# Performance work log

Measured on AMD Instinct MI355X. Metric: run time of the kernel, lower is better.

## Reference

```python
import jax, jax.numpy as jnp
import numpy as np

N, B, NG = 12288, 8, 1536   # total nodes, graphs, nodes per graph
E, T, R, H = 49152, 9, 4, 128  # edges, node types, edge types, hidden

def setup_inputs() -> dict:
    key = jax.random.key(0)
    ks = jax.random.split(key, 24)
    s = 0.05
    inp = {
        'n_feats': jax.random.uniform(ks[0], (N, T), jnp.float32),
        'eps': jax.random.normal(ks[1], (N, H), jnp.float32),
        'edge_src': jax.random.randint(ks[2], (E,), 0, N, jnp.int32),
        'edge_dst': jax.random.randint(ks[3], (E,), 0, N, jnp.int32),
        'e_types': jax.random.randint(ks[4], (E,), 0, R, jnp.int32),
        # RelGraphConv params: per-relation weight, self-loop weight, bias
        'W1': jax.random.normal(ks[5], (R, T, H)) * s,  'Ws1': jax.random.normal(ks[6], (T, H)) * s,  'b1': jnp.zeros((H,)),
        'W2': jax.random.normal(ks[7], (R, H, H)) * s,  'Ws2': jax.random.normal(ks[8], (H, H)) * s,  'b2': jnp.zeros((H,)),
        'Wmu': jax.random.normal(ks[9], (R, H, H)) * s, 'Wsmu': jax.random.normal(ks[10], (H, H)) * s, 'bmu': jnp.zeros((H,)),
        'Wls': jax.random.normal(ks[11], (R, H, H)) * s, 'Wsls': jax.random.normal(ks[12], (H, H)) * s, 'bls': jnp.zeros((H,)),
        # decoder heads
        'Wnt': jax.random.normal(ks[13], (H, T)) * s, 'bnt': jnp.zeros((T,)),
        'we': jax.random.normal(ks[14], (3 * H + 2 * T,)) * s, 'be': jnp.zeros(()),
        'Wt': jax.random.normal(ks[15], (3 * H + 2 * T, R)) * s, 'bt': jnp.zeros((R,)),
    }
    return inp

def _relconv(h, W, Wself, b, edge_src, edge_dst, e_types):
    # per-relation transform then gather per edge: avoids [E,d,d] weight gather
    hr = jnp.einsum('nd,rdk->rnk', h, W)          # [R,N,H]
    msgs = hr[e_types, edge_src]                   # [E,H]
    agg = jax.ops.segment_sum(msgs, edge_dst, num_segments=N)
    return agg + h @ Wself + b

def reference(n_feats, eps, edge_src, edge_dst, e_types,
              W1, Ws1, b1, W2, Ws2, b2, Wmu, Wsmu, bmu, Wls, Wsls, bls,
              Wnt, bnt, we, be, Wt, bt):
    # ---- encode ----
    h = jax.nn.relu(_relconv(n_feats, W1, Ws1, b1, edge_src, edge_dst, e_types))
    h = jax.nn.relu(_relconv(h, W2, Ws2, b2, edge_src, edge_dst, e_types))
    mu = _relconv(h, Wmu, Wsmu, bmu, edge_src, edge_dst, e_types)
    logstd = _relconv(h, Wls, Wsls, bls, edge_src, edge_dst, e_types)
    z = mu + eps * jnp.exp(logstd)                 # reparameterize
    gz = z.reshape(B, NG, H).mean(axis=1)          # per-graph mean readout [B,H]

    # ---- decode (batched pairwise MLP) ----
    nt = z @ Wnt + bnt                             # [N,T]
    # edge_existence_fc on concat(u_z,u_t,v_z,v_t,gz) decomposes rank-1:
    wu_z, wu_t = we[:H], we[H:H + T]
    wv_z, wv_t = we[H + T:2 * H + T], we[2 * H + T:2 * H + 2 * T]
    wg = we[2 * H + 2 * T:]
    su = (z @ wu_z + nt @ wu_t).reshape(B, NG)     # [B,n]
    sv = (z @ wv_z + nt @ wv_t).reshape(B, NG)
    sg = gz @ wg + be                              # [B]
    exist = jax.nn.sigmoid(su[:, :, None] + sv[:, None, :] + sg[:, None, None])  # [B,n,n]

    Au = (z @ Wt[:H] + nt @ Wt[H:H + T]).reshape(B, NG, R)
    Av = (z @ Wt[H + T:2 * H + T] + nt @ Wt[2 * H + T:2 * H + 2 * T]).reshape(B, NG, R)
    Ag = gz @ Wt[2 * H + 2 * T:] + bt              # [B,R]
    type_logits = Au[:, :, None, :] + Av[:, None, :, :] + Ag[:, None, None, :]  # [B,n,n,R]

    pair_out = jnp.concatenate([exist[..., None], type_logits], axis=-1)  # [B,n,n,1+R]
    return pair_out, nt, mu, logstd
```

## Files before the change

### kernel.cpp

```cpp
#include <hip/hip_runtime.h>

#define NN 12288
#define TT 9
#define RR 4
#define HH 128
#define EE 49152
#define BB 8
#define NGG 1536
#define CAP 16

typedef unsigned short u16;
typedef float float4_t __attribute__((ext_vector_type(4)));
typedef __bf16 bf16x8 __attribute__((ext_vector_type(8)));
typedef unsigned short ushort8_t __attribute__((ext_vector_type(8)));

__device__ __forceinline__ u16 f2bf(float f) {
    union { float f; unsigned int u; } x; x.f = f;
    unsigned int r = x.u + 0x7FFFu + ((x.u >> 16) & 1u);
    return (u16)(r >> 16);
}
__device__ __forceinline__ float bf2f(u16 h) {
    union { unsigned int u; float f; } x; x.u = ((unsigned int)h) << 16; return x.f;
}

__global__ __launch_bounds__(256) void build_wts(
    const float* __restrict__ W1, const float* __restrict__ Ws1,
    const float* __restrict__ W2, const float* __restrict__ Ws2,
    const float* __restrict__ Wmu, const float* __restrict__ Wsmu,
    const float* __restrict__ Wls, const float* __restrict__ Wsls,
    u16* __restrict__ Bt1, u16* __restrict__ Bt2, u16* __restrict__ Bt34)
{
    int idx = blockIdx.x * 256 + threadIdx.x;
    if (idx < 128 * 64) {
        int k = idx >> 6, kk = idx & 63;
        float v = 0.f;
        if (kk < 36)      v = W1[kk * HH + k];
        else if (kk < 45) v = Ws1[(kk - 36) * HH + k];
        Bt1[k * 64 + kk] = f2bf(v);
    } else if (idx < 128 * 64 + 128 * 640) {
        int i2 = idx - 128 * 64;
        int k = i2 / 640, kk = i2 - k * 640;
        float v = (kk < 512) ? W2[kk * HH + k] : Ws2[(kk - 512) * HH + k];
        Bt2[k * 640 + kk] = f2bf(v);
    } else if (idx < 128 * 64 + 128 * 640 + 256 * 640) {
        int i3 = idx - (128 * 64 + 128 * 640);
        int j = i3 / 640, kk = i3 - j * 640;
        float v;
        if (j < 128) v = (kk < 512) ? Wmu[kk * HH + j] : Wsmu[(kk - 512) * HH + j];
        else { int jj = j - 128; v = (kk < 512) ? Wls[kk * HH + jj] : Wsls[(kk - 512) * HH + jj]; }
        Bt34[j * 640 + kk] = f2bf(v);
    }
}

__global__ __launch_bounds__(256) void bucket_build(
    const int* __restrict__ esrc, const int* __restrict__ edst,
    const int* __restrict__ etyp, int* __restrict__ cnt, u16* __restrict__ buck)
{
    int e = blockIdx.x * 256 + threadIdx.x;
    if (e >= EE) return;
    int b = edst[e] * RR + etyp[e];
    int idx = atomicAdd(&cnt[b], 1);
    if (idx < CAP) buck[b * CAP + idx] = (u16)esrc[e];
}

__global__ __launch_bounds__(256) void gatherA1(
    const int* __restrict__ cnt, const u16* __restrict__ buck,
    const float* __restrict__ feats, u16* __restrict__ A)
{
    int idx = blockIdx.x * 256 + threadIdx.x;
    int n = idx >> 6, c = idx & 63;
    float v = 0.f;
    if (c < 36) {
        int r = c / 9, t = c - r * 9;
        int b = n * RR + r;
        int m = cnt[b]; m = m > CAP ? CAP : m;
        const u16* bp = buck + b * CAP;
        for (int i = 0; i < m; ++i) v += feats[(int)bp[i] * TT + t];
    } else if (c < 45) {
        v = feats[n * TT + (c - 36)];
    }
    A[(size_t)n * 64 + c] = f2bf(v);
}

__global__ __launch_bounds__(256) void gatherA2(
    const int* __restrict__ cnt, const u16* __restrict__ buck,
    const u16* __restrict__ h, u16* __restrict__ A)
{
    int n = blockIdx.x;
    u16* Ar = A + (size_t)n * 640;
    __shared__ int scnt[RR];
    __shared__ u16 ssrc[RR * CAP];
    if (threadIdx.x < RR) {
        int m = cnt[n * RR + threadIdx.x];
        scnt[threadIdx.x] = m > CAP ? CAP : m;
    }
    if (threadIdx.x < RR * CAP) ssrc[threadIdx.x] = buck[n * RR * CAP + threadIdx.x];
    __syncthreads();
    for (int c = threadIdx.x; c < 640; c += 256) {
        u16 v;
        if (c < 512) {
            int r = c >> 7, k = c & 127;
            float acc = 0.f;
            int m = scnt[r];
            for (int i = 0; i < m; ++i)
                acc += bf2f(h[(size_t)ssrc[r * CAP + i] * HH + k]);
            v = f2bf(acc);
        } else {
            v = h[(size_t)n * HH + (c - 512)];
        }
        Ar[c] = v;
    }
}

template <int MODE>
__global__ __launch_bounds__(256) void gemm_k(
    const u16* __restrict__ A, const u16* __restrict__ Bt, int K,
    const float* __restrict__ bias_a, const float* __restrict__ bias_b,
    u16* __restrict__ outb, float* __restrict__ outf_a, float* __restrict__ outf_b)
{
    __shared__ __align__(16) u16 lds_a[64 * 40];
    __shared__ __align__(16) u16 lds_b[128 * 40];
    const int tid = threadIdx.x;
    const int w = tid >> 6, lane = tid & 63;
    const int m0 = blockIdx.x * 64;
    const int n0 = blockIdx.y * 128;
    const int wm = (w & 1) * 32, wn = (w >> 1) * 64;
    const int lm = lane & 15, lq = lane >> 4;

    float4_t acc[2][4];
#pragma unroll
    for (int i = 0; i < 2; ++i)
#pragma unroll
        for (int j = 0; j < 4; ++j) acc[i][j] = (float4_t){0.f, 0.f, 0.f, 0.f};

    const int arow = tid >> 2, akc = (tid & 3) * 8;
    const int nsteps = K >> 5;
    for (int kt = 0; kt < nsteps; ++kt) {
        int k0 = kt * 32;
        *(ushort8_t*)&lds_a[arow * 40 + akc] =
            *(const ushort8_t*)&A[(size_t)(m0 + arow) * K + k0 + akc];
        {
            int c0 = tid;       int bn0 = c0 >> 2, bk0 = (c0 & 3) * 8;
            *(ushort8_t*)&lds_b[bn0 * 40 + bk0] =
                *(const ushort8_t*)&Bt[(size_t)(n0 + bn0) * K + k0 + bk0];
            int c1 = tid + 256; int bn1 = c1 >> 2, bk1 = (c1 & 3) * 8;
            *(ushort8_t*)&lds_b[bn1 * 40 + bk1] =
                *(const ushort8_t*)&Bt[(size_t)(n0 + bn1) * K + k0 + bk1];
        }
        __syncthreads();
        bf16x8 a0 = *(const bf16x8*)&lds_a[(wm + 0 * 16 + lm) * 40 + lq * 8];
        bf16x8 a1 = *(const bf16x8*)&lds_a[(wm + 1 * 16 + lm) * 40 + lq * 8];
        bf16x8 b0 = *(const bf16x8*)&lds_b[(wn + 0 * 16 + lm) * 40 + lq * 8];
        bf16x8 b1 = *(const bf16x8*)&lds_b[(wn + 1 * 16 + lm) * 40 + lq * 8];
        bf16x8 b2 = *(const bf16x8*)&lds_b[(wn + 2 * 16 + lm) * 40 + lq * 8];
        bf16x8 b3 = *(const bf16x8*)&lds_b[(wn + 3 * 16 + lm) * 40 + lq * 8];
        acc[0][0] = __builtin_amdgcn_mfma_f32_16x16x32_bf16(a0, b0, acc[0][0], 0, 0, 0);
        acc[0][1] = __builtin_amdgcn_mfma_f32_16x16x32_bf16(a0, b1, acc[0][1], 0, 0, 0);
        acc[0][2] = __builtin_amdgcn_mfma_f32_16x16x32_bf16(a0, b2, acc[0][2], 0, 0, 0);
        acc[0][3] = __builtin_amdgcn_mfma_f32_16x16x32_bf16(a0, b3, acc[0][3], 0, 0, 0);
        acc[1][0] = __builtin_amdgcn_mfma_f32_16x16x32_bf16(a1, b0, acc[1][0], 0, 0, 0);
        acc[1][1] = __builtin_amdgcn_mfma_f32_16x16x32_bf16(a1, b1, acc[1][1], 0, 0, 0);
        acc[1][2] = __builtin_amdgcn_mfma_f32_16x16x32_bf16(a1, b2, acc[1][2], 0, 0, 0);
        acc[1][3] = __builtin_amdgcn_mfma_f32_16x16x32_bf16(a1, b3, acc[1][3], 0, 0, 0);
        __syncthreads();
    }

#pragma unroll
    for (int i = 0; i < 2; ++i)
#pragma unroll
        for (int j = 0; j < 4; ++j) {
            int gn = n0 + wn + j * 16 + lm;
#pragma unroll
            for (int reg = 0; reg < 4; ++reg) {
                int gm = m0 + wm + i * 16 + lq * 4 + reg;
                float v = acc[i][j][reg];
                if (MODE == 0) {
                    v += bias_a[gn];
                    v = v > 0.f ? v : 0.f;
                    outb[(size_t)gm * HH + gn] = f2bf(v);
                } else {
                    if (gn < HH) {
                        outf_a[(size_t)gm * HH + gn] = v + bias_a[gn];
                    } else {
                        int g2 = gn - HH;
                        outf_b[(size_t)gm * HH + g2] = v + bias_b[g2];
                    }
                }
            }
        }
}

__global__ __launch_bounds__(256) void z_kernel(
    const float* __restrict__ mu, const float* __restrict__ ls,
    const float* __restrict__ eps, float* __restrict__ z)
{
    int idx = blockIdx.x * 256 + threadIdx.x;
    z[idx] = mu[idx] + eps[idx] * __expf(ls[idx]);
}

__global__ __launch_bounds__(256) void nt_kernel(
    const float* __restrict__ z, const float* __restrict__ Wnt, const float* __restrict__ bnt,
    float* __restrict__ out_nt)
{
    int idx = blockIdx.x * 256 + threadIdx.x;
    if (idx >= NN * TT) return;
    int n = idx / TT, t = idx - n * TT;
    float acc = bnt[t];
    const float* zr = z + (size_t)n * HH;
#pragma unroll 8
    for (int k = 0; k < HH; ++k) acc += zr[k] * Wnt[k * TT + t];
    out_nt[idx] = acc;
}

__global__ __launch_bounds__(256) void nodescalar_kernel(
    const float* __restrict__ z, const float* __restrict__ ntf,
    const float* __restrict__ we, const float* __restrict__ Wt,
    float* __restrict__ su, float* __restrict__ sv,
    float* __restrict__ Au, float* __restrict__ Av)
{
    int n = blockIdx.x * 256 + threadIdx.x;
    const float* zr = z + (size_t)n * HH;
    float s_u = 0, s_v = 0;
    float au[4] = {0, 0, 0, 0}, av[4] = {0, 0, 0, 0};
    for (int k = 0; k < HH; ++k) {
        float zv = zr[k];
        s_u += zv * we[k];
        s_v += zv * we[137 + k];
#pragma unroll
        for (int r = 0; r < 4; ++r) {
            au[r] += zv * Wt[k * 4 + r];
            av[r] += zv * Wt[(137 + k) * 4 + r];
        }
    }
    const float* nr = ntf + (size_t)n * TT;
#pragma unroll
    for (int t = 0; t < TT; ++t) {
        float nv = nr[t];
        s_u += nv * we[128 + t];
        s_v += nv * we[265 + t];
#pragma unroll
        for (int r = 0; r < 4; ++r) {
            au[r] += nv * Wt[(128 + t) * 4 + r];
            av[r] += nv * Wt[(265 + t) * 4 + r];
        }
    }
    su[n] = s_u; sv[n] = s_v;
#pragma unroll
    for (int r = 0; r < 4; ++r) { Au[(size_t)n * 4 + r] = au[r]; Av[(size_t)n * 4 + r] = av[r]; }
}

__global__ __launch_bounds__(256) void gz_part_kernel(
    const float* __restrict__ z, float* __restrict__ part)
{
    int b = blockIdx.x >> 5, chunk = blockIdx.x & 31;
    int k = threadIdx.x & 127, half = threadIdx.x >> 7;
    const float* zb = z + ((size_t)b * NGG + chunk * 48 + half * 24) * HH + k;
    float s = 0.f;
#pragma unroll 8
    for (int g = 0; g < 24; ++g) s += zb[(size_t)g * HH];
    __shared__ float red[256];
    red[threadIdx.x] = s;
    __syncthreads();
    if (threadIdx.x < 128)
        part[((size_t)b * 32 + chunk) * 128 + k] = red[threadIdx.x] + red[threadIdx.x + 128];
}

__global__ __launch_bounds__(128) void gz_final_kernel(
    const float* __restrict__ part, const float* __restrict__ we,
    const float* __restrict__ Wt, const float* __restrict__ be,
    const float* __restrict__ bt, float* __restrict__ sg, float* __restrict__ Ag)
{
    int b = blockIdx.x, k = threadIdx.x;
    float s = 0.f;
#pragma unroll 8
    for (int c = 0; c < 32; ++c) s += part[((size_t)b * 32 + c) * 128 + k];
    float gz = s * (1.f / NGG);
    float vals[5] = { we[274 + k], Wt[(274 + k) * 4 + 0], Wt[(274 + k) * 4 + 1],
                      Wt[(274 + k) * 4 + 2], Wt[(274 + k) * 4 + 3] };
    __shared__ float red[128];
    for (int j = 0; j < 5; ++j) {
        red[k] = gz * vals[j];
        __syncthreads();
        for (int off = 64; off >= 1; off >>= 1) {
            if (k < off) red[k] += red[k + off];
            __syncthreads();
        }
        if (k == 0) {
            if (j == 0) sg[b] = red[0] + be[0];
            else        Ag[b * 4 + (j - 1)] = red[0] + bt[j - 1];
        }
        __syncthreads();
    }
}

__global__ __launch_bounds__(256) void pair_kernel(
    const float* __restrict__ su, const float* __restrict__ sv,
    const float* __restrict__ Au, const float* __restrict__ Av,
    const float* __restrict__ sg, const float* __restrict__ Ag,
    float* __restrict__ out)
{
    int row = blockIdx.x;
    int b = row / NGG;
    float su_u = su[row] + sg[b];
    float t0 = Au[(size_t)row * 4 + 0] + Ag[b * 4 + 0];
    float t1 = Au[(size_t)row * 4 + 1] + Ag[b * 4 + 1];
    float t2 = Au[(size_t)row * 4 + 2] + Ag[b * 4 + 2];
    float t3 = Au[(size_t)row * 4 + 3] + Ag[b * 4 + 3];
    const float* svb = sv + (size_t)b * NGG;
    const float* avb = Av + (size_t)b * NGG * 4;
    float4_t* od = (float4_t*)(out + (size_t)row * 7680);
    for (int d = threadIdx.x; d < 1920; d += 256) {
        float4_t vv;
#pragma unroll
        for (int j = 0; j < 4; ++j) {
            unsigned int e = (unsigned int)d * 4u + j;
            unsigned int v0 = (e * 52429u) >> 18;
            unsigned int c  = e - v0 * 5u;
            float f;
            if (c == 0u) { float x = su_u + svb[v0]; f = 1.f / (1.f + __expf(-x)); }
            else { float tv = (c == 1u) ? t0 : (c == 2u) ? t1 : (c == 3u) ? t2 : t3;
                   f = tv + avb[v0 * 4u + (c - 1u)]; }
            vv[j] = f;
        }
        od[d] = vv;
    }
}

extern "C" void kernel_launch(void* const* d_in, const int* in_sizes, int n_in,
                              void* d_out, int out_size, void* d_ws, size_t ws_size,
                              hipStream_t stream)
{
    const float* feats = (const float*)d_in[0];
    const float* eps   = (const float*)d_in[1];
    const int* esrc  = (const int*)d_in[2];
    const int* edst  = (const int*)d_in[3];
    const int* etyp  = (const int*)d_in[4];
    const float* W1    = (const float*)d_in[5];
    const float* Ws1   = (const float*)d_in[6];
    const float* b1    = (const float*)d_in[7];
    const float* W2    = (const float*)d_in[8];
    const float* Ws2   = (const float*)d_in[9];
    const float* b2    = (const float*)d_in[10];
    const float* Wmu   = (const float*)d_in[11];
    const float* Wsmu  = (const float*)d_in[12];
    const float* bmu   = (const float*)d_in[13];
    const float* Wls   = (const float*)d_in[14];
    const float* Wsls  = (const float*)d_in[15];
    const float* bls   = (const float*)d_in[16];
    const float* Wnt   = (const float*)d_in[17];
    const float* bnt   = (const float*)d_in[18];
    const float* we    = (const float*)d_in[19];
    const float* be    = (const float*)d_in[20];
    const float* Wt    = (const float*)d_in[21];
    const float* bt    = (const float*)d_in[22];

    char* p = (char*)d_ws;
    auto alloc = [&](size_t bytes) -> char* {
        char* r = p; p += (bytes + 255) & ~(size_t)255; return r;
    };
    u16*   Abuf  = (u16*)  alloc((size_t)NN * 640 * 2);
    u16*   hbf   = (u16*)  alloc((size_t)NN * HH * 2);
    float* zf    = (float*)alloc((size_t)NN * HH * 4);
    int*   cnt   = (int*)  alloc((size_t)NN * RR * 4);
    u16*   buck  = (u16*)  alloc((size_t)NN * RR * CAP * 2);
    float* part  = (float*)alloc((size_t)BB * 32 * 128 * 4);
    u16*   Bt1   = (u16*)  alloc(128 * 64 * 2);
    u16*   Bt2   = (u16*)  alloc(128 * 640 * 2);
    u16*   Bt34  = (u16*)  alloc(256 * 640 * 2);
    float* suA   = (float*)alloc(NN * 4);
    float* svA   = (float*)alloc(NN * 4);
    float* AuA   = (float*)alloc(NN * 4 * 4);
    float* AvA   = (float*)alloc(NN * 4 * 4);
    float* sgA   = (float*)alloc(BB * 4);
    float* AgA   = (float*)alloc(BB * 4 * 4);

    float* out = (float*)d_out;
    const size_t PO = (size_t)BB * NGG * NGG * 5;
    float* out_nt = out + PO;
    float* out_mu = out_nt + (size_t)NN * TT;
    float* out_ls = out_mu + (size_t)NN * HH;

    build_wts<<<992, 256, 0, stream>>>(W1, Ws1, W2, Ws2, Wmu, Wsmu, Wls, Wsls, Bt1, Bt2, Bt34);

    hipMemsetAsync(cnt, 0, (size_t)NN * RR * 4, stream);
    bucket_build<<<EE / 256, 256, 0, stream>>>(esrc, edst, etyp, cnt, buck);

    gatherA1<<<NN * 64 / 256, 256, 0, stream>>>(cnt, buck, feats, Abuf);
    gemm_k<0><<<dim3(NN / 64, 1), 256, 0, stream>>>(Abuf, Bt1, 64, b1, nullptr,
                                                    hbf, nullptr, nullptr);

    gatherA2<<<NN, 256, 0, stream>>>(cnt, buck, hbf, Abuf);
    gemm_k<0><<<dim3(NN / 64, 1), 256, 0, stream>>>(Abuf, Bt2, 640, b2, nullptr,
                                                    hbf, nullptr, nullptr);

    gatherA2<<<NN, 256, 0, stream>>>(cnt, buck, hbf, Abuf);
    gemm_k<1><<<dim3(NN / 64, 2), 256, 0, stream>>>(Abuf, Bt34, 640, bmu, bls,
                                                    nullptr, out_mu, out_ls);

    z_kernel<<<NN * HH / 256, 256, 0, stream>>>(out_mu, out_ls, eps, zf);
    nt_kernel<<<(NN * TT + 255) / 256, 256, 0, stream>>>(zf, Wnt, bnt, out_nt);
    nodescalar_kernel<<<NN / 256, 256, 0, stream>>>(zf, out_nt, we, Wt, suA, svA, AuA, AvA);
    gz_part_kernel<<<BB * 32, 256, 0, stream>>>(zf, part);
    gz_final_kernel<<<BB, 128, 0, stream>>>(part, we, Wt, be, bt, sgA, AgA);
    pair_kernel<<<NN, 256, 0, stream>>>(suA, svA, AuA, AvA, sgA, AgA, out);
}
```

Baseline: 618.5 us.

## Fuse node epilogue kernels, fold memset into weight build, nontemporal pair stores

Merges the z computation, nt projection, per-node scalar heads and the per-graph partial mean into one kernel that keeps z for 64 nodes in shared memory, so the fp32 z buffer never goes to global memory. The graph-mean partials are accumulated with atomics into a small buffer, which build_wts now zeroes along with the bucket counters, replacing the separate memset. The large pair output is written with nontemporal stores to avoid cache pollution. Atomic float accumulation makes the order of summation nondeterministic.

New measurement: 602.9 us. -2.5%, faster.

```diff
diff --git a/kernel.cpp b/kernel.cpp
--- a/kernel.cpp
+++ b/kernel.cpp
@@ -28,27 +28,37 @@
     const float* __restrict__ W2, const float* __restrict__ Ws2,
     const float* __restrict__ Wmu, const float* __restrict__ Wsmu,
     const float* __restrict__ Wls, const float* __restrict__ Wsls,
-    u16* __restrict__ Bt1, u16* __restrict__ Bt2, u16* __restrict__ Bt34)
-{
+    u16* __restrict__ Bt1, u16* __restrict__ Bt2, u16* __restrict__ Bt34,
+    int* __restrict__ cnt, float* __restrict__ gzacc)
+{
+    const int L1 = 128 * 64;
+    const int L2 = L1 + 128 * 640;
+    const int L3 = L2 + 256 * 640;
+    const int L4 = L3 + NN * RR;
+    const int L5 = L4 + BB * HH;
     int idx = blockIdx.x * 256 + threadIdx.x;
-    if (idx < 128 * 64) {
+    if (idx < L1) {
         int k = idx >> 6, kk = idx & 63;
         float v = 0.f;
         if (kk < 36)      v = W1[kk * HH + k];
         else if (kk < 45) v = Ws1[(kk - 36) * HH + k];
         Bt1[k * 64 + kk] = f2bf(v);
-    } else if (idx < 128 * 64 + 128 * 640) {
-        int i2 = idx - 128 * 64;
+    } else if (idx < L2) {
+        int i2 = idx - L1;
         int k = i2 / 640, kk = i2 - k * 640;
         float v = (kk < 512) ? W2[kk * HH + k] : Ws2[(kk - 512) * HH + k];
         Bt2[k * 640 + kk] = f2bf(v);
-    } else if (idx < 128 * 64 + 128 * 640 + 256 * 640) {
-        int i3 = idx - (128 * 64 + 128 * 640);
+    } else if (idx < L3) {
+        int i3 = idx - L2;
         int j = i3 / 640, kk = i3 - j * 640;
         float v;
         if (j < 128) v = (kk < 512) ? Wmu[kk * HH + j] : Wsmu[(kk - 512) * HH + j];
         else { int jj = j - 128; v = (kk < 512) ? Wls[kk * HH + jj] : Wsls[(kk - 512) * HH + jj]; }
         Bt34[j * 640 + kk] = f2bf(v);
+    } else if (idx < L4) {
+        cnt[idx - L3] = 0;
+    } else if (idx < L5) {
+        gzacc[idx - L4] = 0.f;
     }
 }
 
@@ -190,91 +200,86 @@
         }
 }
 
-__global__ __launch_bounds__(256) void z_kernel(
+__global__ __launch_bounds__(256) void node_epi(
     const float* __restrict__ mu, const float* __restrict__ ls,
-    const float* __restrict__ eps, float* __restrict__ z)
-{
-    int idx = blockIdx.x * 256 + threadIdx.x;
-    z[idx] = mu[idx] + eps[idx] * __expf(ls[idx]);
-}
-
-__global__ __launch_bounds__(256) void nt_kernel(
-    const float* __restrict__ z, const float* __restrict__ Wnt, const float* __restrict__ bnt,
-    float* __restrict__ out_nt)
-{
-    int idx = blockIdx.x * 256 + threadIdx.x;
-    if (idx >= NN * TT) return;
-    int n = idx / TT, t = idx - n * TT;
-    float acc = bnt[t];
-    const float* zr = z + (size_t)n * HH;
+    const float* __restrict__ eps,
+    const float* __restrict__ Wnt, const float* __restrict__ bnt,
+    const float* __restrict__ we, const float* __restrict__ Wt,
+    float* __restrict__ out_nt,
+    float* __restrict__ su, float* __restrict__ sv,
+    float* __restrict__ Au, float* __restrict__ Av,
+    float* __restrict__ gzacc)
+{
+    __shared__ float zs[64][129];
+    __shared__ float nts[64][10];
+    __shared__ float red[256];
+    const int nb = blockIdx.x * 64;
+    const int tid = threadIdx.x;
+
+    for (int i = tid; i < 64 * 32; i += 256) {
+        int n = i >> 5, c4 = (i & 31) * 4;
+        size_t g = (size_t)(nb + n) * HH + c4;
+        float4_t m4 = *(const float4_t*)&mu[g];
+        float4_t l4 = *(const float4_t*)&ls[g];
+        float4_t e4 = *(const float4_t*)&eps[g];
+        float* zp = &zs[n][c4];
+#pragma unroll
+        for (int j = 0; j < 4; ++j) zp[j] = m4[j] + e4[j] * __expf(l4[j]);
+    }
+    __syncthreads();
+
+    for (int o = tid; o < 64 * TT; o += 256) {
+        int n = o / TT, t = o - n * TT;
+        float acc = bnt[t];
 #pragma unroll 8
-    for (int k = 0; k < HH; ++k) acc += zr[k] * Wnt[k * TT + t];
-    out_nt[idx] = acc;
-}
-
-__global__ __launch_bounds__(256) void nodescalar_kernel(
-    const float* __restrict__ z, const float* __restrict__ ntf,
-    const float* __restrict__ we, const float* __restrict__ Wt,
-    float* __restrict__ su, float* __restrict__ sv,
-    float* __restrict__ Au, float* __restrict__ Av)
-{
-    int n = blockIdx.x * 256 + threadIdx.x;
-    const float* zr = z + (size_t)n * HH;
-    float s_u = 0, s_v = 0;
-    float au[4] = {0, 0, 0, 0}, av[4] = {0, 0, 0, 0};
-    for (int k = 0; k < HH; ++k) {
-        float zv = zr[k];
-        s_u += zv * we[k];
-        s_v += zv * we[137 + k];
-#pragma unroll
-        for (int r = 0; r < 4; ++r) {
-            au[r] += zv * Wt[k * 4 + r];
-            av[r] += zv * Wt[(137 + k) * 4 + r];
-        }
-    }
-    const float* nr = ntf + (size_t)n * TT;
-#pragma unroll
-    for (int t = 0; t < TT; ++t) {
-        float nv = nr[t];
-        s_u += nv * we[128 + t];
-        s_v += nv * we[265 + t];
-#pragma unroll
-        for (int r = 0; r < 4; ++r) {
-            au[r] += nv * Wt[(128 + t) * 4 + r];
-            av[r] += nv * Wt[(265 + t) * 4 + r];
-        }
-    }
-    su[n] = s_u; sv[n] = s_v;
-#pragma unroll
-    for (int r = 0; r < 4; ++r) { Au[(size_t)n * 4 + r] = au[r]; Av[(size_t)n * 4 + r] = av[r]; }
-}
-
-__global__ __launch_bounds__(256) void gz_part_kernel(
-    const float* __restrict__ z, float* __restrict__ part)
-{
-    int b = blockIdx.x >> 5, chunk = blockIdx.x & 31;
-    int k = threadIdx.x & 127, half = threadIdx.x >> 7;
-    const float* zb = z + ((size_t)b * NGG + chunk * 48 + half * 24) * HH + k;
-    float s = 0.f;
+        for (int k = 0; k < HH; ++k) acc += zs[n][k] * Wnt[k * TT + t];
+        nts[n][t] = acc;
+        out_nt[(size_t)(nb + n) * TT + t] = acc;
+    }
+    __syncthreads();
+
+    for (int o = tid; o < 64 * 10; o += 256) {
+        int n = o / 10, j = o - n * 10;
+        int zoff, toff;
+        const float* wv;
+        if (j == 0)      { zoff = 0;   toff = 128; wv = we; }
+        else if (j == 1) { zoff = 137; toff = 265; wv = we; }
+        else if (j < 6)  { zoff = 0;   toff = 128; wv = Wt + (j - 2); }
+        else             { zoff = 137; toff = 265; wv = Wt + (j - 6); }
+        int stride = (j < 2) ? 1 : 4;
+        float acc = 0.f;
 #pragma unroll 8
-    for (int g = 0; g < 24; ++g) s += zb[(size_t)g * HH];
-    __shared__ float red[256];
-    red[threadIdx.x] = s;
-    __syncthreads();
-    if (threadIdx.x < 128)
-        part[((size_t)b * 32 + chunk) * 128 + k] = red[threadIdx.x] + red[threadIdx.x + 128];
+        for (int k = 0; k < HH; ++k) acc += zs[n][k] * wv[(zoff + k) * stride];
+#pragma unroll
+        for (int t = 0; t < TT; ++t) acc += nts[n][t] * wv[(toff + t) * stride];
+        int gn = nb + n;
+        if (j == 0)      su[gn] = acc;
+        else if (j == 1) sv[gn] = acc;
+        else if (j < 6)  Au[(size_t)gn * 4 + (j - 2)] = acc;
+        else             Av[(size_t)gn * 4 + (j - 6)] = acc;
+    }
+
+    {
+        int k = tid & 127, half = tid >> 7;
+        float s = 0.f;
+#pragma unroll 8
+        for (int r = 0; r < 32; ++r) s += zs[half * 32 + r][k];
+        red[tid] = s;
+        __syncthreads();
+        if (tid < 128) {
+            int b = blockIdx.x / 24;
+            atomicAdd(&gzacc[b * HH + tid], red[tid] + red[tid + 128]);
+        }
+    }
 }
 
 __global__ __launch_bounds__(128) void gz_final_kernel(
-    const float* __restrict__ part, const float* __restrict__ we,
+    const float* __restrict__ gzacc, const float* __restrict__ we,
     const float* __restrict__ Wt, const float* __restrict__ be,
     const float* __restrict__ bt, float* __restrict__ sg, float* __restrict__ Ag)
 {
     int b = blockIdx.x, k = threadIdx.x;
-    float s = 0.f;
-#pragma unroll 8
-    for (int c = 0; c < 32; ++c) s += part[((size_t)b * 32 + c) * 128 + k];
-    float gz = s * (1.f / NGG);
+    float gz = gzacc[b * HH + k] * (1.f / NGG);
     float vals[5] = { we[274 + k], Wt[(274 + k) * 4 + 0], Wt[(274 + k) * 4 + 1],
                       Wt[(274 + k) * 4 + 2], Wt[(274 + k) * 4 + 3] };
     __shared__ float red[128];
@@ -322,7 +327,7 @@
                    f = tv + avb[v0 * 4u + (c - 1u)]; }
             vv[j] = f;
         }
-        od[d] = vv;
+        __builtin_nontemporal_store(vv, &od[d]);
     }
 }
 
@@ -360,10 +365,9 @@
     };
     u16*   Abuf  = (u16*)  alloc((size_t)NN * 640 * 2);
     u16*   hbf   = (u16*)  alloc((size_t)NN * HH * 2);
-    float* zf    = (float*)alloc((size_t)NN * HH * 4);
     int*   cnt   = (int*)  alloc((size_t)NN * RR * 4);
     u16*   buck  = (u16*)  alloc((size_t)NN * RR * CAP * 2);
-    float* part  = (float*)alloc((size_t)BB * 32 * 128 * 4);
+    float* gzacc = (float*)alloc((size_t)BB * HH * 4);
     u16*   Bt1   = (u16*)  alloc(128 * 64 * 2);
     u16*   Bt2   = (u16*)  alloc(128 * 640 * 2);
     u16*   Bt34  = (u16*)  alloc(256 * 640 * 2);
@@ -380,9 +384,9 @@
     float* out_mu = out_nt + (size_t)NN * TT;
     float* out_ls = out_mu + (size_t)NN * HH;
 
-    build_wts<<<992, 256, 0, stream>>>(W1, Ws1, W2, Ws2, Wmu, Wsmu, Wls, Wsls, Bt1, Bt2, Bt34);
-
-    hipMemsetAsync(cnt, 0, (size_t)NN * RR * 4, stream);
+    build_wts<<<1188, 256, 0, stream>>>(W1, Ws1, W2, Ws2, Wmu, Wsmu, Wls, Wsls,
+                                        Bt1, Bt2, Bt34, cnt, gzacc);
+
     bucket_build<<<EE / 256, 256, 0, stream>>>(esrc, edst, etyp, cnt, buck);
 
     gatherA1<<<NN * 64 / 256, 256, 0, stream>>>(cnt, buck, feats, Abuf);
@@ -397,10 +401,9 @@
     gemm_k<1><<<dim3(NN / 64, 2), 256, 0, stream>>>(Abuf, Bt34, 640, bmu, bls,
                                                     nullptr, out_mu, out_ls);
 
-    z_kernel<<<NN * HH / 256, 256, 0, stream>>>(out_mu, out_ls, eps, zf);
-    nt_kernel<<<(NN * TT + 255) / 256, 256, 0, stream>>>(zf, Wnt, bnt, out_nt);
-    nodescalar_kernel<<<NN / 256, 256, 0, stream>>>(zf, out_nt, we, Wt, suA, svA, AuA, AvA);
-    gz_part_kernel<<<BB * 32, 256, 0, stream>>>(zf, part);
-    gz_final_kernel<<<BB, 128, 0, stream>>>(part, we, Wt, be, bt, sgA, AgA);
+    node_epi<<<NN / 64, 256, 0, stream>>>(out_mu, out_ls, eps, Wnt, bnt, we, Wt,
+                                          out_nt, suA, svA, AuA, AvA, gzacc);
+
+    gz_final_kernel<<<BB, 128, 0, stream>>>(gzacc, we, Wt, be, bt, sgA, AgA);
     pair_kernel<<<NN, 256, 0, stream>>>(suA, svA, AuA, AvA, sgA, AgA, out);
 }
```
